# Performance work log

Measured on AMD Instinct MI355X. Metric: run time of the kernel, lower is better.

The kernel has to match this reference:

```python
import jax, jax.numpy as jnp
import numpy as np

B, T, F = 32, 2048, 16
C = F + 1      # input channels (time prepended)
H = 64         # output_dims: latent CDE state size
HH = 64        # hidden_dims: vector-field MLP width
DEPTH = 4      # num_hidden_layers -> DEPTH-1 inner linears
INIT = 64      # intial_dims


def _lin(k, fan_in, shape):
    b = 1.0 / np.sqrt(fan_in)
    return jax.random.uniform(k, shape, jnp.float32, -b, b)


def setup_inputs() -> dict:
    key = jax.random.key(0)
    ks = jax.random.split(key, 15)
    return {
        "x": jax.random.normal(ks[0], (B, T, F), jnp.float32),
        # z0 initializer MLP: Linear(C,INIT) -> ReLU -> Linear(INIT,H)
        "wi1": _lin(ks[1], C, (C, INIT)), "bi1": _lin(ks[2], C, (INIT,)),
        "wi2": _lin(ks[3], INIT, (INIT, H)), "bi2": _lin(ks[4], INIT, (H,)),
        # CDEFunc
        "w_in": _lin(ks[5], H, (H, HH)), "b_in": _lin(ks[6], H, (HH,)),
        "w_hid": _lin(ks[7], HH, (DEPTH - 1, HH, HH)), "b_hid": _lin(ks[8], HH, (DEPTH - 1, HH)),
        "w_out": _lin(ks[9], HH, (HH, C * H)), "b_out": _lin(ks[10], HH, (C * H,)),
        # output projection Linear(H, F)
        "w_proj": _lin(ks[11], H, (H, F)), "b_proj": _lin(ks[12], H, (F,)),
    }


def _cde_f(z, w_in, b_in, w_hid, b_hid, w_out, b_out):
    # CDEFunc.forward: MLP -> tanh, reshaped to (b, H, C)
    h = jax.nn.relu(z @ w_in + b_in)
    for i in range(w_hid.shape[0]):
        h = jax.nn.relu(h @ w_hid[i] + b_hid[i])
    return jnp.tanh((h @ w_out + b_out).reshape(z.shape[0], H, C))


def _forward(x, wi1, bi1, wi2, bi2, w_in, b_in, w_hid, b_hid, w_out, b_out, w_proj, b_proj):
    b, t_len, _ = x.shape
    t = jnp.arange(t_len, dtype=x.dtype)
    xa = jnp.concatenate([jnp.broadcast_to(t[None, :, None], (b, t_len, 1)), x], axis=-1)  # (b,T,C)

    # Hermite cubic with backward differences (torchcde): knot derivs are backward
    # diffs with the first repeated; on interval i (h=1):
    #   X'(s) = d_i + 2*c_i*s + 3*e_i*s^2,  c_i = 3*dx - 2*d_i - d_{i+1},  e_i = -2*dx + d_i + d_{i+1}
    diffs = xa[:, 1:] - xa[:, :-1]                      # (b,T-1,C)
    d = jnp.concatenate([diffs[:, :1], diffs], axis=1)  # (b,T,C)
    di, dip1 = d[:, :-1], d[:, 1:]
    cc = 3.0 * diffs - 2.0 * di - dip1
    ee = -2.0 * diffs + di + dip1

    def deriv(s):
        return di + (2.0 * s) * cc + (3.0 * s * s) * ee  # (b,T-1,C)

    # torchdiffeq 'rk4' = 3/8-rule: evals at s = 0, 1/3, 2/3, 1 within each unit interval
    xdots = jnp.stack([deriv(0.0), deriv(1.0 / 3.0), deriv(2.0 / 3.0), deriv(1.0)], axis=0)
    xdots = jnp.moveaxis(xdots, 2, 0)  # (T-1, 4, b, C)

    z0 = jax.nn.relu(xa[:, 0] @ wi1 + bi1) @ wi2 + bi2  # (b,H)

    def g(z, xd):
        f = _cde_f(z, w_in, b_in, w_hid, b_hid, w_out, b_out)  # (b,H,C)
        return jnp.einsum('bhc,bc->bh', f, xd)

    def step(z, xd4):
        k1 = g(z, xd4[0])
        k2 = g(z + k1 / 3.0, xd4[1])
        k3 = g(z + (k2 - k1 / 3.0), xd4[2])
        k4 = g(z + (k1 - k2 + k3), xd4[3])
        zn = z + (k1 + 3.0 * (k2 + k3) + k4) * 0.125
        return zn, zn

    _, zs = jax.lax.scan(step, z0, xdots)                # (T-1,b,H)
    z_T = jnp.moveaxis(jnp.concatenate([z0[None], zs], axis=0), 0, 1)  # (b,T,H)

    # act -> dropout (eval: identity) -> output_layer
    out = jax.nn.gelu(z_T, approximate=False) @ w_proj + b_proj        # (b,T,F)
    return z_T, out


def reference(x, wi1, bi1, wi2, bi2, w_in, b_in, w_hid, b_hid, w_out, b_out, w_proj, b_proj):
    z_T, out = _forward(x, wi1, bi1, wi2, bi2, w_in, b_in, w_hid, b_hid, w_out, b_out, w_proj, b_proj)
    not_mask = jnp.zeros((x.shape[0], x.shape[1]), dtype=bool)  # mask='all_true' (eval mode)
    return z_T, out, not_mask
```

## Files before the change

### kernel.cpp

```cpp
#include <hip/hip_runtime.h>
#include <math.h>

#define BB 32
#define TT 2048
#define FF 16
#define CC 17
#define HH 64

typedef float v2f __attribute__((ext_vector_type(2)));
typedef float v4f __attribute__((ext_vector_type(4)));

__device__ __forceinline__ float rl(float v, int lane) {
    return __int_as_float(__builtin_amdgcn_readlane(__float_as_int(v), lane));
}

__device__ __forceinline__ float ftanh(float x) {
    float e = __builtin_amdgcn_exp2f(x * 2.88539008177792681472f);
    return 1.0f - 2.0f * __builtin_amdgcn_rcpf(e + 1.0f);
}

#define PIN(v) asm volatile("" : "+v"(v))
#define PIN2(v) do { double _d = __builtin_bit_cast(double, v); \
                     asm volatile("" : "+v"(_d));               \
                     v = __builtin_bit_cast(v2f, _d); } while (0)

__attribute__((amdgpu_waves_per_eu(2, 2)))
__launch_bounds__(512)
__global__ void ncde_main(const float* __restrict__ x,
                          const float* __restrict__ wi1, const float* __restrict__ bi1,
                          const float* __restrict__ wi2, const float* __restrict__ bi2,
                          const float* __restrict__ w_in, const float* __restrict__ b_in,
                          const float* __restrict__ w_hid, const float* __restrict__ b_hid,
                          const float* __restrict__ w_out, const float* __restrict__ b_out,
                          float* __restrict__ zT)
{
    const int b   = blockIdx.x;
    const int tid = threadIdx.x;
    const int w   = tid >> 6;
    const int l   = tid & 63;

    __shared__ float ph[4][8][64];
    __shared__ __align__(16) float hbuf[64];
    __shared__ v2f  pgq[8][64];

    float whid[4][8];
    #pragma unroll
    for (int kk = 0; kk < 8; ++kk) {
        int k = 8 * w + kk;
        whid[0][kk] = w_in[k * HH + l];
        whid[1][kk] = w_hid[(0 * HH + k) * HH + l];
        whid[2][kk] = w_hid[(1 * HH + k) * HH + l];
        whid[3][kk] = w_hid[(2 * HH + k) * HH + l];
    }
    float bfold[4];
    bfold[0] = (w == 0) ? b_in[l] : 0.0f;
    bfold[1] = (w == 0) ? b_hid[0 * HH + l] : 0.0f;
    bfold[2] = (w == 0) ? b_hid[1 * HH + l] : 0.0f;
    bfold[3] = (w == 0) ? b_hid[2 * HH + l] : 0.0f;

    const int c0 = 2 * w, c1 = 2 * w + 1;
    v2f wopk[64];
    #pragma unroll
    for (int k = 0; k < 64; ++k) {
        wopk[k].x = w_out[k * (CC * HH) + l * CC + c0];
        wopk[k].y = w_out[k * (CC * HH) + l * CC + c1];
    }
    float w16[8];
    #pragma unroll
    for (int kk = 0; kk < 8; ++kk)
        w16[kk] = w_out[(8 * w + kk) * (CC * HH) + l * CC + 16];
    float bo0   = b_out[l * CC + c0];
    float bo1   = b_out[l * CC + c1];
    float bo16f = (w == 0) ? b_out[l * CC + 16] : 0.0f;

    #pragma unroll
    for (int k = 0; k < 64; ++k) PIN2(wopk[k]);
    #pragma unroll
    for (int kk = 0; kk < 8; ++kk) {
        PIN(w16[kk]);
        PIN(whid[0][kk]); PIN(whid[1][kk]); PIN(whid[2][kk]); PIN(whid[3][kk]);
    }
    #pragma unroll
    for (int i = 0; i < 4; ++i) PIN(bfold[i]);
    PIN(bo0); PIN(bo1); PIN(bo16f);

    float h0 = bi1[l];
    #pragma unroll
    for (int c = 1; c < CC; ++c) {
        float xc = x[(b * TT + 0) * FF + (c - 1)];
        h0 = fmaf(xc, wi1[c * HH + l], h0);
    }
    h0 = fmaxf(h0, 0.0f);
    float z = bi2[l];
    #pragma unroll
    for (int k = 0; k < 64; ++k)
        z = fmaf(rl(h0, k), wi2[k * HH + l], z);

    if (w == 0) zT[(b * TT + 0) * HH + l] = z;

    auto G = [&](float zin, float xd0, float xd1, float xd16) -> float {
        float cur = zin;
        #pragma unroll
        for (int layer = 0; layer < 4; ++layer) {
            float a0 = bfold[layer], a1 = 0.0f;
            #pragma unroll
            for (int kk = 0; kk < 8; kk += 2) {
                float s0 = rl(cur, 8 * w + kk);
                float s1 = rl(cur, 8 * w + kk + 1);
                a0 = fmaf(s0, whid[layer][kk],     a0);
                a1 = fmaf(s1, whid[layer][kk + 1], a1);
            }
            ph[layer][w][l] = a0 + a1;
            __syncthreads();
            float r0 = ph[layer][0][l], r1 = ph[layer][1][l];
            float r2 = ph[layer][2][l], r3 = ph[layer][3][l];
            float r4 = ph[layer][4][l], r5 = ph[layer][5][l];
            float r6 = ph[layer][6][l], r7 = ph[layer][7][l];
            float nx = ((r0 + r1) + (r2 + r3)) + ((r4 + r5) + (r6 + r7));
            cur = fmaxf(nx, 0.0f);
        }
        if (w == 0) hbuf[l] = cur;
        __syncthreads();

        v2f u0 = { bo0, bo1 }, u1 = { 0.f, 0.f }, u2 = { 0.f, 0.f }, u3 = { 0.f, 0.f };
        #pragma unroll
        for (int j = 0; j < 16; ++j) {
            v4f q = *reinterpret_cast<const v4f*>(&hbuf[4 * j]);
            u0 += wopk[4 * j + 0] * q.x;
            u1 += wopk[4 * j + 1] * q.y;
            u2 += wopk[4 * j + 2] * q.z;
            u3 += wopk[4 * j + 3] * q.w;
        }
        v2f ut = (u0 + u1) + (u2 + u3);

        v4f qa = *reinterpret_cast<const v4f*>(&hbuf[8 * w]);
        v4f qb = *reinterpret_cast<const v4f*>(&hbuf[8 * w + 4]);
        float a16a = bo16f, a16b = 0.0f;
        a16a = fmaf(qa.x, w16[0], a16a); a16b = fmaf(qa.y, w16[1], a16b);
        a16a = fmaf(qa.z, w16[2], a16a); a16b = fmaf(qa.w, w16[3], a16b);
        a16a = fmaf(qb.x, w16[4], a16a); a16b = fmaf(qb.y, w16[5], a16b);
        a16a = fmaf(qb.z, w16[6], a16a); a16b = fmaf(qb.w, w16[7], a16b);

        float pg = ftanh(ut.x) * xd0 + ftanh(ut.y) * xd1;
        pgq[w][l] = (v2f){ pg, a16a + a16b };
        __syncthreads();
        v2f s0 = pgq[0][l], s1 = pgq[1][l], s2 = pgq[2][l], s3 = pgq[3][l];
        v2f s4 = pgq[4][l], s5 = pgq[5][l], s6 = pgq[6][l], s7 = pgq[7][l];
        v2f st = ((s0 + s1) + (s2 + s3)) + ((s4 + s5) + (s6 + s7));
        return fmaf(ftanh(st.y), xd16, st.x);
    };

    const float* xb = x + (size_t)b * TT * FF;
    const bool hasc0 = (w != 0);
    const int  f0 = 2 * w - 1;
    const int  f1 = 2 * w;
    float xp0 = hasc0 ? xb[0 * FF + f0] : 0.0f;
    float xp1 = xb[0 * FF + f1];
    float xp16 = xb[0 * FF + 15];
    float xn0 = hasc0 ? xb[1 * FF + f0] : 0.0f;
    float xn1 = xb[1 * FF + f1];
    float xn16 = xb[1 * FF + 15];
    float dc0 = hasc0 ? (xn0 - xp0) : 1.0f;
    float dc1 = xn1 - xp1;
    float dc16 = xn16 - xp16;
    float dp0 = dc0, dp1 = dc1, dp16 = dc16;
    xp0 = xn0; xp1 = xn1; xp16 = xn16;

    #pragma unroll 1
    for (int t = 0; t < TT - 1; ++t) {
        const float f43 = 4.0f / 3.0f;
        float x20  = dp0  + f43 * (dc0  - dp0);
        float x21  = dp1  + f43 * (dc1  - dp1);
        float x216 = dp16 + f43 * (dc16 - dp16);

        int tn = (t + 2 < TT) ? (t + 2) : (TT - 1);
        float yn0 = hasc0 ? xb[tn * FF + f0] : 0.0f;
        float yn1 = xb[tn * FF + f1];
        float yn16 = xb[tn * FF + 15];

        float k1 = G(z, dp0, dp1, dp16);
        float k2 = G(z + k1 * (1.0f / 3.0f), dc0, dc1, dc16);
        float k3 = G(z + (k2 - k1 * (1.0f / 3.0f)), x20, x21, x216);
        float k4 = G(z + (k1 - k2 + k3), dc0, dc1, dc16);
        z = z + 0.125f * (k1 + 3.0f * (k2 + k3) + k4);

        if (w == 0) zT[(b * TT + (t + 1)) * HH + l] = z;

        dp0 = dc0; dp1 = dc1; dp16 = dc16;
        dc0 = hasc0 ? (yn0 - xp0) : 1.0f;
        dc1 = yn1 - xp1;
        dc16 = yn16 - xp16;
        xp0 = yn0; xp1 = yn1; xp16 = yn16;
    }
}

__global__ void ncde_proj(const float* __restrict__ zT,
                          const float* __restrict__ w_proj, const float* __restrict__ b_proj,
                          float* __restrict__ out, float* __restrict__ mask)
{
    __shared__ float gz[16][64];
    const int blk = blockIdx.x;
    const int tid = threadIdx.x;
    const int r16 = tid >> 4, f = tid & 15;
    const int row0 = blk * 16;

    #pragma unroll
    for (int i = 0; i < 4; ++i) {
        int idx = tid + i * 256;
        int r = idx >> 6, k = idx & 63;
        float zv = zT[(size_t)(row0 + r) * HH + k];
        gz[r][k] = 0.5f * zv * (1.0f + erff(zv * 0.70710678118654752f));
    }
    __syncthreads();

    float acc = b_proj[f];
    #pragma unroll
    for (int k = 0; k < 64; ++k)
        acc = fmaf(gz[r16][k], w_proj[k * FF + f], acc);
    out[(size_t)(row0 + r16) * FF + f] = acc;
    if (f == 0) mask[row0 + r16] = 0.0f;
}

extern "C" void kernel_launch(void* const* d_in, const int* in_sizes, int n_in,
                              void* d_out, int out_size, void* d_ws, size_t ws_size,
                              hipStream_t stream)
{
    (void)in_sizes; (void)n_in; (void)d_ws; (void)ws_size; (void)out_size;
    const float* x      = (const float*)d_in[0];
    const float* wi1    = (const float*)d_in[1];
    const float* bi1    = (const float*)d_in[2];
    const float* wi2    = (const float*)d_in[3];
    const float* bi2    = (const float*)d_in[4];
    const float* w_in   = (const float*)d_in[5];
    const float* b_in   = (const float*)d_in[6];
    const float* w_hid  = (const float*)d_in[7];
    const float* b_hid  = (const float*)d_in[8];
    const float* w_out  = (const float*)d_in[9];
    const float* b_out  = (const float*)d_in[10];
    const float* w_proj = (const float*)d_in[11];
    const float* b_proj = (const float*)d_in[12];

    float* zT   = (float*)d_out;
    float* outp = zT + (size_t)BB * TT * HH;
    float* mask = outp + (size_t)BB * TT * FF;

    ncde_main<<<dim3(BB), dim3(512), 0, stream>>>(
        x, wi1, bi1, wi2, bi2, w_in, b_in, w_hid, b_hid, w_out, b_out, zT);
    ncde_proj<<<dim3((BB * TT) / 16), dim3(256), 0, stream>>>(
        zT, w_proj, b_proj, outp, mask);
}
```

Measured before the change: 13.28 ms.

## Pack output-layer weights to fp16 dot2 and move hidden weights to LDS

The output-layer weights are stored as packed fp16 pairs and multiplied with v_dot2 against a pre-scaled fp16 copy of the hidden vector. This halves the register footprint and the number of multiply instructions in the largest matvec. The hidden-layer weights move from registers into shared memory and are reloaded each layer, and the x loads are made wave-uniform with readfirstlane. The costs are reduced precision in the w_out product, with an fp16 overflow/underflow risk that the 1/256 scaling is meant to control, plus extra LDS traffic on the serial critical path.

```diff
diff --git a/kernel.cpp b/kernel.cpp
--- a/kernel.cpp
+++ b/kernel.cpp
@@ -9,20 +9,33 @@
 
 typedef float v2f __attribute__((ext_vector_type(2)));
 typedef float v4f __attribute__((ext_vector_type(4)));
+typedef unsigned int v4u __attribute__((ext_vector_type(4)));
+typedef _Float16 h2 __attribute__((ext_vector_type(2)));
 
 __device__ __forceinline__ float rl(float v, int lane) {
     return __int_as_float(__builtin_amdgcn_readlane(__float_as_int(v), lane));
 }
-
+__device__ __forceinline__ float uf(float v) {
+    return __int_as_float(__builtin_amdgcn_readfirstlane(__float_as_int(v)));
+}
 __device__ __forceinline__ float ftanh(float x) {
     float e = __builtin_amdgcn_exp2f(x * 2.88539008177792681472f);
     return 1.0f - 2.0f * __builtin_amdgcn_rcpf(e + 1.0f);
 }
+__device__ __forceinline__ float fdot2(unsigned int a, unsigned int b, float c) {
+    h2 ha = __builtin_bit_cast(h2, a), hb = __builtin_bit_cast(h2, b);
+#if __has_builtin(__builtin_amdgcn_fdot2)
+    return __builtin_amdgcn_fdot2(ha, hb, c, false);
+#else
+    return fmaf((float)ha.x, (float)hb.x, fmaf((float)ha.y, (float)hb.y, c));
+#endif
+}
+__device__ __forceinline__ unsigned int packf16(float a, float b) {
+    h2 p; p.x = (_Float16)a; p.y = (_Float16)b;
+    return __builtin_bit_cast(unsigned int, p);
+}
 
 #define PIN(v) asm volatile("" : "+v"(v))
-#define PIN2(v) do { double _d = __builtin_bit_cast(double, v); \
-                     asm volatile("" : "+v"(_d));               \
-                     v = __builtin_bit_cast(v2f, _d); } while (0)
 
 __attribute__((amdgpu_waves_per_eu(2, 2)))
 __launch_bounds__(512)
@@ -39,19 +52,17 @@
     const int w   = tid >> 6;
     const int l   = tid & 63;
 
+    __shared__ float Wl[4][64][64];
     __shared__ float ph[4][8][64];
-    __shared__ __align__(16) float hbuf[64];
+    __shared__ __align__(16) unsigned int hb16[32];
     __shared__ v2f  pgq[8][64];
 
-    float whid[4][8];
-    #pragma unroll
-    for (int kk = 0; kk < 8; ++kk) {
-        int k = 8 * w + kk;
-        whid[0][kk] = w_in[k * HH + l];
-        whid[1][kk] = w_hid[(0 * HH + k) * HH + l];
-        whid[2][kk] = w_hid[(1 * HH + k) * HH + l];
-        whid[3][kk] = w_hid[(2 * HH + k) * HH + l];
-    }
+    {
+        float* wl = (float*)Wl;
+        for (int i = tid; i < 64 * 64; i += 512)     wl[i] = w_in[i];
+        for (int i = tid; i < 3 * 64 * 64; i += 512) wl[64 * 64 + i] = w_hid[i];
+    }
+
     float bfold[4];
     bfold[0] = (w == 0) ? b_in[l] : 0.0f;
     bfold[1] = (w == 0) ? b_hid[0 * HH + l] : 0.0f;
@@ -59,30 +70,28 @@
     bfold[3] = (w == 0) ? b_hid[2 * HH + l] : 0.0f;
 
     const int c0 = 2 * w, c1 = 2 * w + 1;
-    v2f wopk[64];
-    #pragma unroll
-    for (int k = 0; k < 64; ++k) {
-        wopk[k].x = w_out[k * (CC * HH) + l * CC + c0];
-        wopk[k].y = w_out[k * (CC * HH) + l * CC + c1];
-    }
-    float w16[8];
-    #pragma unroll
-    for (int kk = 0; kk < 8; ++kk)
-        w16[kk] = w_out[(8 * w + kk) * (CC * HH) + l * CC + 16];
-    float bo0   = b_out[l * CC + c0];
-    float bo1   = b_out[l * CC + c1];
-    float bo16f = (w == 0) ? b_out[l * CC + 16] : 0.0f;
-
-    #pragma unroll
-    for (int k = 0; k < 64; ++k) PIN2(wopk[k]);
-    #pragma unroll
-    for (int kk = 0; kk < 8; ++kk) {
-        PIN(w16[kk]);
-        PIN(whid[0][kk]); PIN(whid[1][kk]); PIN(whid[2][kk]); PIN(whid[3][kk]);
-    }
-    #pragma unroll
-    for (int i = 0; i < 4; ++i) PIN(bfold[i]);
-    PIN(bo0); PIN(bo1); PIN(bo16f);
+    unsigned int wo0p[32], wo1p[32], w16p[4];
+    #pragma unroll
+    for (int j = 0; j < 32; ++j) {
+        wo0p[j] = packf16(w_out[(2 * j) * (CC * HH) + l * CC + c0],
+                          w_out[(2 * j + 1) * (CC * HH) + l * CC + c0]);
+        wo1p[j] = packf16(w_out[(2 * j) * (CC * HH) + l * CC + c1],
+                          w_out[(2 * j + 1) * (CC * HH) + l * CC + c1]);
+    }
+    #pragma unroll
+    for (int j = 0; j < 4; ++j)
+        w16p[j] = packf16(w_out[(8 * w + 2 * j) * (CC * HH) + l * CC + 16],
+                          w_out[(8 * w + 2 * j + 1) * (CC * HH) + l * CC + 16]);
+    float bo0  = b_out[l * CC + c0];
+    float bo1  = b_out[l * CC + c1];
+    float bo16 = b_out[l * CC + 16];
+
+    #pragma unroll
+    for (int j = 0; j < 32; ++j) { PIN(wo0p[j]); PIN(wo1p[j]); }
+    #pragma unroll
+    for (int j = 0; j < 4; ++j) PIN(w16p[j]);
+
+    __syncthreads();
 
     float h0 = bi1[l];
     #pragma unroll
@@ -102,66 +111,78 @@
         float cur = zin;
         #pragma unroll
         for (int layer = 0; layer < 4; ++layer) {
+            float wk0 = Wl[layer][8 * w + 0][l], wk1 = Wl[layer][8 * w + 1][l];
+            float wk2 = Wl[layer][8 * w + 2][l], wk3 = Wl[layer][8 * w + 3][l];
+            float wk4 = Wl[layer][8 * w + 4][l], wk5 = Wl[layer][8 * w + 5][l];
+            float wk6 = Wl[layer][8 * w + 6][l], wk7 = Wl[layer][8 * w + 7][l];
             float a0 = bfold[layer], a1 = 0.0f;
-            #pragma unroll
-            for (int kk = 0; kk < 8; kk += 2) {
-                float s0 = rl(cur, 8 * w + kk);
-                float s1 = rl(cur, 8 * w + kk + 1);
-                a0 = fmaf(s0, whid[layer][kk],     a0);
-                a1 = fmaf(s1, whid[layer][kk + 1], a1);
-            }
+            a0 = fmaf(rl(cur, 8 * w + 0), wk0, a0);
+            a1 = fmaf(rl(cur, 8 * w + 1), wk1, a1);
+            a0 = fmaf(rl(cur, 8 * w + 2), wk2, a0);
+            a1 = fmaf(rl(cur, 8 * w + 3), wk3, a1);
+            a0 = fmaf(rl(cur, 8 * w + 4), wk4, a0);
+            a1 = fmaf(rl(cur, 8 * w + 5), wk5, a1);
+            a0 = fmaf(rl(cur, 8 * w + 6), wk6, a0);
+            a1 = fmaf(rl(cur, 8 * w + 7), wk7, a1);
             ph[layer][w][l] = a0 + a1;
             __syncthreads();
             float r0 = ph[layer][0][l], r1 = ph[layer][1][l];
             float r2 = ph[layer][2][l], r3 = ph[layer][3][l];
             float r4 = ph[layer][4][l], r5 = ph[layer][5][l];
             float r6 = ph[layer][6][l], r7 = ph[layer][7][l];
-            float nx = ((r0 + r1) + (r2 + r3)) + ((r4 + r5) + (r6 + r7));
-            cur = fmaxf(nx, 0.0f);
+            cur = fmaxf(((r0 + r1) + (r2 + r3)) + ((r4 + r5) + (r6 + r7)), 0.0f);
         }
-        if (w == 0) hbuf[l] = cur;
+        float pm = __shfl_xor(cur, 1);
+        if (w == 0 && (l & 1) == 0)
+            hb16[l >> 1] = __builtin_bit_cast(unsigned int,
+                __builtin_amdgcn_cvt_pkrtz(cur * 0.00390625f, pm * 0.00390625f));
         __syncthreads();
 
-        v2f u0 = { bo0, bo1 }, u1 = { 0.f, 0.f }, u2 = { 0.f, 0.f }, u3 = { 0.f, 0.f };
+        float u0a = 0.f, u0b = 0.f, u0c = 0.f, u0d = 0.f;
+        float u1a = 0.f, u1b = 0.f, u1c = 0.f, u1d = 0.f;
         #pragma unroll
-        for (int j = 0; j < 16; ++j) {
-            v4f q = *reinterpret_cast<const v4f*>(&hbuf[4 * j]);
-            u0 += wopk[4 * j + 0] * q.x;
-            u1 += wopk[4 * j + 1] * q.y;
-            u2 += wopk[4 * j + 2] * q.z;
-            u3 += wopk[4 * j + 3] * q.w;
+        for (int j = 0; j < 8; ++j) {
+            v4u q = *reinterpret_cast<const v4u*>(&hb16[4 * j]);
+            u0a = fdot2(q.x, wo0p[4 * j + 0], u0a);
+            u0b = fdot2(q.y, wo0p[4 * j + 1], u0b);
+            u0c = fdot2(q.z, wo0p[4 * j + 2], u0c);
+            u0d = fdot2(q.w, wo0p[4 * j + 3], u0d);
+            u1a = fdot2(q.x, wo1p[4 * j + 0], u1a);
+            u1b = fdot2(q.y, wo1p[4 * j + 1], u1b);
+            u1c = fdot2(q.z, wo1p[4 * j + 2], u1c);
+            u1d = fdot2(q.w, wo1p[4 * j + 3], u1d);
         }
-        v2f ut = (u0 + u1) + (u2 + u3);
-
-        v4f qa = *reinterpret_cast<const v4f*>(&hbuf[8 * w]);
-        v4f qb = *reinterpret_cast<const v4f*>(&hbuf[8 * w + 4]);
-        float a16a = bo16f, a16b = 0.0f;
-        a16a = fmaf(qa.x, w16[0], a16a); a16b = fmaf(qa.y, w16[1], a16b);
-        a16a = fmaf(qa.z, w16[2], a16a); a16b = fmaf(qa.w, w16[3], a16b);
-        a16a = fmaf(qb.x, w16[4], a16a); a16b = fmaf(qb.y, w16[5], a16b);
-        a16a = fmaf(qb.z, w16[6], a16a); a16b = fmaf(qb.w, w16[7], a16b);
-
-        float pg = ftanh(ut.x) * xd0 + ftanh(ut.y) * xd1;
+        float u0 = fmaf(((u0a + u0b) + (u0c + u0d)), 256.0f, bo0);
+        float u1 = fmaf(((u1a + u1b) + (u1c + u1d)), 256.0f, bo1);
+
+        v4u qc = *reinterpret_cast<const v4u*>(&hb16[4 * w]);
+        float a16a = fdot2(qc.x, w16p[0], 0.0f);
+        float a16b = fdot2(qc.y, w16p[1], 0.0f);
+        a16a = fdot2(qc.z, w16p[2], a16a);
+        a16b = fdot2(qc.w, w16p[3], a16b);
+
+        float pg = ftanh(u0) * xd0 + ftanh(u1) * xd1;
         pgq[w][l] = (v2f){ pg, a16a + a16b };
         __syncthreads();
         v2f s0 = pgq[0][l], s1 = pgq[1][l], s2 = pgq[2][l], s3 = pgq[3][l];
         v2f s4 = pgq[4][l], s5 = pgq[5][l], s6 = pgq[6][l], s7 = pgq[7][l];
         v2f st = ((s0 + s1) + (s2 + s3)) + ((s4 + s5) + (s6 + s7));
-        return fmaf(ftanh(st.y), xd16, st.x);
+        float u16 = fmaf(st.y, 256.0f, bo16);
+        return fmaf(ftanh(u16), xd16, st.x);
     };
 
     const float* xb = x + (size_t)b * TT * FF;
     const bool hasc0 = (w != 0);
     const int  f0 = 2 * w - 1;
     const int  f1 = 2 * w;
-    float xp0 = hasc0 ? xb[0 * FF + f0] : 0.0f;
-    float xp1 = xb[0 * FF + f1];
-    float xp16 = xb[0 * FF + 15];
-    float xn0 = hasc0 ? xb[1 * FF + f0] : 0.0f;
-    float xn1 = xb[1 * FF + f1];
-    float xn16 = xb[1 * FF + 15];
-    float dc0 = hasc0 ? (xn0 - xp0) : 1.0f;
-    float dc1 = xn1 - xp1;
+    float xp0  = hasc0 ? uf(xb[0 * FF + f0]) : 0.0f;
+    float xp1  = uf(xb[0 * FF + f1]);
+    float xp16 = uf(xb[0 * FF + 15]);
+    float xn0  = hasc0 ? uf(xb[1 * FF + f0]) : 0.0f;
+    float xn1  = uf(xb[1 * FF + f1]);
+    float xn16 = uf(xb[1 * FF + 15]);
+    float dc0  = hasc0 ? (xn0 - xp0) : 1.0f;
+    float dc1  = xn1 - xp1;
     float dc16 = xn16 - xp16;
     float dp0 = dc0, dp1 = dc1, dp16 = dc16;
     xp0 = xn0; xp1 = xn1; xp16 = xn16;
@@ -174,9 +195,9 @@
         float x216 = dp16 + f43 * (dc16 - dp16);
 
         int tn = (t + 2 < TT) ? (t + 2) : (TT - 1);
-        float yn0 = hasc0 ? xb[tn * FF + f0] : 0.0f;
-        float yn1 = xb[tn * FF + f1];
-        float yn16 = xb[tn * FF + 15];
+        float yn0  = hasc0 ? uf(xb[tn * FF + f0]) : 0.0f;
+        float yn1  = uf(xb[tn * FF + f1]);
+        float yn16 = uf(xb[tn * FF + 15]);
 
         float k1 = G(z, dp0, dp1, dp16);
         float k2 = G(z + k1 * (1.0f / 3.0f), dc0, dc1, dc16);
```

After: 14.31 ms. +7.8%, slower.

## Use packed fp16 dot2 for output layer with readlane broadcast, drop LDS hbuf barrier

Applied to the files above, without the earlier changes.

Stores the w_out weights as packed fp16 pairs and computes the output layer with v_dot2 (fp16 inputs, fp32 accumulation). The hidden vector is scaled by 1/256 so it stays in fp16 range, packed with a shuffle, and broadcast from lanes with readlane. This removes the hbuf LDS round trip and one barrier per vector-field evaluation. Barriers become explicit lgkmcnt-wait plus s_barrier, and x loads go through readfirstlane. Weight register pressure roughly halves, but fp16 rounding of weights and activations can hurt accuracy over the 2047-step recurrence.

```diff
diff --git a/kernel.cpp b/kernel.cpp
--- a/kernel.cpp
+++ b/kernel.cpp
@@ -8,21 +8,33 @@
 #define HH 64
 
 typedef float v2f __attribute__((ext_vector_type(2)));
-typedef float v4f __attribute__((ext_vector_type(4)));
+typedef _Float16 h2 __attribute__((ext_vector_type(2)));
 
 __device__ __forceinline__ float rl(float v, int lane) {
     return __int_as_float(__builtin_amdgcn_readlane(__float_as_int(v), lane));
 }
-
+__device__ __forceinline__ int rli(int v, int lane) {
+    return __builtin_amdgcn_readlane(v, lane);
+}
+__device__ __forceinline__ float uf(float v) {
+    return __int_as_float(__builtin_amdgcn_readfirstlane(__float_as_int(v)));
+}
 __device__ __forceinline__ float ftanh(float x) {
     float e = __builtin_amdgcn_exp2f(x * 2.88539008177792681472f);
     return 1.0f - 2.0f * __builtin_amdgcn_rcpf(e + 1.0f);
 }
-
+__device__ __forceinline__ float fdot2u(unsigned a, unsigned b, float c) {
+    return __builtin_amdgcn_fdot2(__builtin_bit_cast(h2, a),
+                                  __builtin_bit_cast(h2, b), c, false);
+}
+__device__ __forceinline__ unsigned packf16(float a, float b) {
+    h2 p; p.x = (_Float16)a; p.y = (_Float16)b;
+    return __builtin_bit_cast(unsigned, p);
+}
+__device__ __forceinline__ void bar_lds() {
+    asm volatile("s_waitcnt lgkmcnt(0)\n\ts_barrier" ::: "memory");
+}
 #define PIN(v) asm volatile("" : "+v"(v))
-#define PIN2(v) do { double _d = __builtin_bit_cast(double, v); \
-                     asm volatile("" : "+v"(_d));               \
-                     v = __builtin_bit_cast(v2f, _d); } while (0)
 
 __attribute__((amdgpu_waves_per_eu(2, 2)))
 __launch_bounds__(512)
@@ -40,7 +52,6 @@
     const int l   = tid & 63;
 
     __shared__ float ph[4][8][64];
-    __shared__ __align__(16) float hbuf[64];
     __shared__ v2f  pgq[8][64];
 
     float whid[4][8];
@@ -59,44 +70,51 @@
     bfold[3] = (w == 0) ? b_hid[2 * HH + l] : 0.0f;
 
     const int c0 = 2 * w, c1 = 2 * w + 1;
-    v2f wopk[64];
-    #pragma unroll
-    for (int k = 0; k < 64; ++k) {
-        wopk[k].x = w_out[k * (CC * HH) + l * CC + c0];
-        wopk[k].y = w_out[k * (CC * HH) + l * CC + c1];
-    }
-    float w16[8];
-    #pragma unroll
-    for (int kk = 0; kk < 8; ++kk)
-        w16[kk] = w_out[(8 * w + kk) * (CC * HH) + l * CC + 16];
-    float bo0   = b_out[l * CC + c0];
-    float bo1   = b_out[l * CC + c1];
-    float bo16f = (w == 0) ? b_out[l * CC + 16] : 0.0f;
-
-    #pragma unroll
-    for (int k = 0; k < 64; ++k) PIN2(wopk[k]);
-    #pragma unroll
-    for (int kk = 0; kk < 8; ++kk) {
-        PIN(w16[kk]);
-        PIN(whid[0][kk]); PIN(whid[1][kk]); PIN(whid[2][kk]); PIN(whid[3][kk]);
-    }
-    #pragma unroll
-    for (int i = 0; i < 4; ++i) PIN(bfold[i]);
-    PIN(bo0); PIN(bo1); PIN(bo16f);
-
-    float h0 = bi1[l];
-    #pragma unroll
-    for (int c = 1; c < CC; ++c) {
-        float xc = x[(b * TT + 0) * FF + (c - 1)];
-        h0 = fmaf(xc, wi1[c * HH + l], h0);
-    }
-    h0 = fmaxf(h0, 0.0f);
-    float z = bi2[l];
-    #pragma unroll
-    for (int k = 0; k < 64; ++k)
-        z = fmaf(rl(h0, k), wi2[k * HH + l], z);
-
-    if (w == 0) zT[(b * TT + 0) * HH + l] = z;
+    unsigned wo0p[32], wo1p[32], w16p[4];
+    #pragma unroll
+    for (int j = 0; j < 32; ++j) {
+        wo0p[j] = packf16(w_out[(2 * j) * (CC * HH) + l * CC + c0],
+                          w_out[(2 * j + 1) * (CC * HH) + l * CC + c0]);
+        wo1p[j] = packf16(w_out[(2 * j) * (CC * HH) + l * CC + c1],
+                          w_out[(2 * j + 1) * (CC * HH) + l * CC + c1]);
+    }
+    #pragma unroll
+    for (int jj = 0; jj < 4; ++jj)
+        w16p[jj] = packf16(w_out[(8 * w + 2 * jj) * (CC * HH) + l * CC + 16],
+                           w_out[(8 * w + 2 * jj + 1) * (CC * HH) + l * CC + 16]);
+    float bo0  = b_out[l * CC + c0];
+    float bo1  = b_out[l * CC + c1];
+    float bo16 = b_out[l * CC + 16];
+
+    #pragma unroll
+    for (int j = 0; j < 32; ++j) { PIN(wo0p[j]); PIN(wo1p[j]); }
+    #pragma unroll
+    for (int jj = 0; jj < 4; ++jj) PIN(w16p[jj]);
+    #pragma unroll
+    for (int i = 0; i < 4; ++i) { PIN(bfold[i]); }
+    PIN(bo0); PIN(bo1); PIN(bo16);
+
+    float z;
+    {
+        float h0 = bi1[l];
+        #pragma unroll
+        for (int c = 1; c < CC; ++c)
+            h0 = fmaf(x[(size_t)b * TT * FF + (c - 1)], wi1[c * HH + l], h0);
+        h0 = fmaxf(h0, 0.0f);
+        z = bi2[l];
+        #pragma unroll
+        for (int k = 0; k < 64; ++k)
+            z = fmaf(rl(h0, k), wi2[k * HH + l], z);
+    }
+    if (w == 0) zT[(size_t)b * TT * HH + l] = z;
+
+    auto packb = [&](float hval) -> unsigned {
+        float hs = hval * 0.00390625f;
+        float pr = __shfl_xor(hs, 1);
+        float a  = (l & 1) ? pr : hs;
+        float bb = (l & 1) ? hs : pr;
+        return __builtin_bit_cast(unsigned, __builtin_amdgcn_cvt_pkrtz(a, bb));
+    };
 
     auto G = [&](float zin, float xd0, float xd1, float xd16) -> float {
         float cur = zin;
@@ -111,57 +129,56 @@
                 a1 = fmaf(s1, whid[layer][kk + 1], a1);
             }
             ph[layer][w][l] = a0 + a1;
-            __syncthreads();
+            bar_lds();
             float r0 = ph[layer][0][l], r1 = ph[layer][1][l];
             float r2 = ph[layer][2][l], r3 = ph[layer][3][l];
             float r4 = ph[layer][4][l], r5 = ph[layer][5][l];
             float r6 = ph[layer][6][l], r7 = ph[layer][7][l];
-            float nx = ((r0 + r1) + (r2 + r3)) + ((r4 + r5) + (r6 + r7));
-            cur = fmaxf(nx, 0.0f);
+            cur = fmaxf(((r0 + r1) + (r2 + r3)) + ((r4 + r5) + (r6 + r7)), 0.0f);
         }
-        if (w == 0) hbuf[l] = cur;
-        __syncthreads();
-
-        v2f u0 = { bo0, bo1 }, u1 = { 0.f, 0.f }, u2 = { 0.f, 0.f }, u3 = { 0.f, 0.f };
-        #pragma unroll
-        for (int j = 0; j < 16; ++j) {
-            v4f q = *reinterpret_cast<const v4f*>(&hbuf[4 * j]);
-            u0 += wopk[4 * j + 0] * q.x;
-            u1 += wopk[4 * j + 1] * q.y;
-            u2 += wopk[4 * j + 2] * q.z;
-            u3 += wopk[4 * j + 3] * q.w;
+        unsigned hp = packb(cur);
+        float u0a = 0.f, u0b = 0.f, u1a = 0.f, u1b = 0.f;
+        #pragma unroll
+        for (int j = 0; j < 32; j += 2) {
+            unsigned s0 = (unsigned)rli((int)hp, 2 * j);
+            unsigned s1 = (unsigned)rli((int)hp, 2 * j + 2);
+            u0a = fdot2u(s0, wo0p[j],     u0a);
+            u1a = fdot2u(s0, wo1p[j],     u1a);
+            u0b = fdot2u(s1, wo0p[j + 1], u0b);
+            u1b = fdot2u(s1, wo1p[j + 1], u1b);
         }
-        v2f ut = (u0 + u1) + (u2 + u3);
-
-        v4f qa = *reinterpret_cast<const v4f*>(&hbuf[8 * w]);
-        v4f qb = *reinterpret_cast<const v4f*>(&hbuf[8 * w + 4]);
-        float a16a = bo16f, a16b = 0.0f;
-        a16a = fmaf(qa.x, w16[0], a16a); a16b = fmaf(qa.y, w16[1], a16b);
-        a16a = fmaf(qa.z, w16[2], a16a); a16b = fmaf(qa.w, w16[3], a16b);
-        a16a = fmaf(qb.x, w16[4], a16a); a16b = fmaf(qb.y, w16[5], a16b);
-        a16a = fmaf(qb.z, w16[6], a16a); a16b = fmaf(qb.w, w16[7], a16b);
-
-        float pg = ftanh(ut.x) * xd0 + ftanh(ut.y) * xd1;
+        float a16a = 0.f, a16b = 0.f;
+        #pragma unroll
+        for (int jj = 0; jj < 4; jj += 2) {
+            unsigned s0 = (unsigned)rli((int)hp, 8 * w + 2 * jj);
+            unsigned s1 = (unsigned)rli((int)hp, 8 * w + 2 * jj + 2);
+            a16a = fdot2u(s0, w16p[jj],     a16a);
+            a16b = fdot2u(s1, w16p[jj + 1], a16b);
+        }
+        float u0 = fmaf(u0a + u0b, 256.0f, bo0);
+        float u1 = fmaf(u1a + u1b, 256.0f, bo1);
+        float pg = ftanh(u0) * xd0 + ftanh(u1) * xd1;
         pgq[w][l] = (v2f){ pg, a16a + a16b };
-        __syncthreads();
+        bar_lds();
         v2f s0 = pgq[0][l], s1 = pgq[1][l], s2 = pgq[2][l], s3 = pgq[3][l];
         v2f s4 = pgq[4][l], s5 = pgq[5][l], s6 = pgq[6][l], s7 = pgq[7][l];
         v2f st = ((s0 + s1) + (s2 + s3)) + ((s4 + s5) + (s6 + s7));
-        return fmaf(ftanh(st.y), xd16, st.x);
+        float u16 = fmaf(st.y, 256.0f, bo16);
+        return fmaf(ftanh(u16), xd16, st.x);
     };
 
     const float* xb = x + (size_t)b * TT * FF;
     const bool hasc0 = (w != 0);
     const int  f0 = 2 * w - 1;
     const int  f1 = 2 * w;
-    float xp0 = hasc0 ? xb[0 * FF + f0] : 0.0f;
-    float xp1 = xb[0 * FF + f1];
-    float xp16 = xb[0 * FF + 15];
-    float xn0 = hasc0 ? xb[1 * FF + f0] : 0.0f;
-    float xn1 = xb[1 * FF + f1];
-    float xn16 = xb[1 * FF + 15];
-    float dc0 = hasc0 ? (xn0 - xp0) : 1.0f;
-    float dc1 = xn1 - xp1;
+    float xp0  = hasc0 ? uf(xb[f0]) : 0.0f;
+    float xp1  = uf(xb[f1]);
+    float xp16 = uf(xb[15]);
+    float xn0  = hasc0 ? uf(xb[FF + f0]) : 0.0f;
+    float xn1  = uf(xb[FF + f1]);
+    float xn16 = uf(xb[FF + 15]);
+    float dc0  = hasc0 ? (xn0 - xp0) : 1.0f;
+    float dc1  = xn1 - xp1;
     float dc16 = xn16 - xp16;
     float dp0 = dc0, dp1 = dc1, dp16 = dc16;
     xp0 = xn0; xp1 = xn1; xp16 = xn16;
@@ -174,9 +191,9 @@
         float x216 = dp16 + f43 * (dc16 - dp16);
 
         int tn = (t + 2 < TT) ? (t + 2) : (TT - 1);
-        float yn0 = hasc0 ? xb[tn * FF + f0] : 0.0f;
-        float yn1 = xb[tn * FF + f1];
-        float yn16 = xb[tn * FF + 15];
+        float yn0  = hasc0 ? uf(xb[tn * FF + f0]) : 0.0f;
+        float yn1  = uf(xb[tn * FF + f1]);
+        float yn16 = uf(xb[tn * FF + 15]);
 
         float k1 = G(z, dp0, dp1, dp16);
         float k2 = G(z + k1 * (1.0f / 3.0f), dc0, dc1, dc16);
@@ -184,7 +201,7 @@
         float k4 = G(z + (k1 - k2 + k3), dc0, dc1, dc16);
         z = z + 0.125f * (k1 + 3.0f * (k2 + k3) + k4);
 
-        if (w == 0) zT[(b * TT + (t + 1)) * HH + l] = z;
+        if (w == 0) zT[((size_t)b * TT + t + 1) * HH + l] = z;
 
         dp0 = dc0; dp1 = dc1; dp16 = dc16;
         dc0 = hasc0 ? (yn0 - xp0) : 1.0f;
```

After: 13.12 ms. About the same (-1.2%).
